# Optimization experiments

Hardware: AMD Instinct MI355X
Metric: run time of the kernel (lower is better)

The kernel has to match this reference:

```python
import jax, jax.numpy as jnp
import numpy as np

D_MODEL = 512
NHEAD = 8


def setup_inputs() -> dict:
    key = jax.random.key(0)
    ks = jax.random.split(key, 8)
    d = D_MODEL
    low_feats = jax.random.normal(ks[0], (1, d, 32, 32), dtype=jnp.float32)
    guide_feats = jax.random.normal(ks[1], (1, d, 128, 128), dtype=jnp.float32)
    s = 1.0 / np.sqrt(d)
    Wq = jax.random.normal(ks[2], (d, d), dtype=jnp.float32) * s
    Wk = jax.random.normal(ks[3], (d, d), dtype=jnp.float32) * s
    Wv = jax.random.normal(ks[4], (d, d), dtype=jnp.float32) * s
    Wm = jax.random.normal(ks[5], (d, d), dtype=jnp.float32) * s
    gamma = jnp.ones((d,), dtype=jnp.float32)
    beta = jnp.zeros((d,), dtype=jnp.float32)
    return {"low_feats": low_feats, "guide_feats": guide_feats, "Wq": Wq,
            "Wk": Wk, "Wv": Wv, "Wm": Wm, "gamma": gamma, "beta": beta}


def _gather_windows(feat_hw, H, W):
    # feat_hw: [b, h, w, nhead, dim]. For each guide pixel (Y,X), nearest low
    # pixel is (Y*h//H, X*w//W) (PyTorch 'nearest'); gather its 3x3 neighborhood
    # with replicate padding (index clamping). Window order = ky*3+kx, matching
    # F.unfold channel layout. Returns [b, H*W, 9, nhead, dim].
    b, h, w, nh, dm = feat_hw.shape
    offs = jnp.array([-1, 0, 1])
    y0 = jnp.arange(H) * h // H                      # [H]
    x0 = jnp.arange(W) * w // W                      # [W]
    ys = jnp.clip(y0[:, None] + offs, 0, h - 1)      # [H,3] (ky)
    xs = jnp.clip(x0[:, None] + offs, 0, w - 1)      # [W,3] (kx)
    # -> [b, H, W, 3(ky), 3(kx), nhead, dim]
    g = feat_hw[:, ys[:, None, :, None], xs[None, :, None, :]]
    return g.reshape(b, H * W, 9, nh, dm)


def reference(low_feats, guide_feats, Wq, Wk, Wv, Wm, gamma, beta):
    b, d, H, W = guide_feats.shape
    _, _, h, w = low_feats.shape
    nh = NHEAD
    dm = d // nh
    g = guide_feats.transpose(0, 2, 3, 1).reshape(b, H * W, d)
    l = low_feats.transpose(0, 2, 3, 1).reshape(b, h * w, d)
    q = (g @ Wq.T).reshape(b, H * W, nh, dm)                 # [b,N,h,d]
    K = (l @ Wk.T).reshape(b, h, w, nh, dm)
    V = (l @ Wv.T).reshape(b, h, w, nh, dm)
    key = _gather_windows(K, H, W)                           # [b,N,9,h,d]
    val = _gather_windows(V, H, W)
    scale = 1.0 / jnp.sqrt(jnp.asarray(dm, dtype=q.dtype))
    # (q/sqrt(dm)) @ (k/sqrt(dm)) * sqrt(dm) == q@k / sqrt(dm)
    score = jnp.einsum('bnhd,bnkhd->bnhk', q, key) * scale
    attn = jax.nn.softmax(score, axis=-1)
    msg = jnp.einsum('bnhk,bnkhd->bnhd', attn, val).reshape(b, H * W, d)
    msg = msg @ Wm.T
    # LayerNorm(d_model), eps=1e-5
    mu = jnp.mean(msg, axis=-1, keepdims=True)
    var = jnp.mean((msg - mu) ** 2, axis=-1, keepdims=True)
    msg = (msg - mu) * jax.lax.rsqrt(var + 1e-5) * gamma + beta
    return msg.transpose(0, 2, 1).reshape(b, d, H, W)
```

## Files before the change

kernel.cpp:

```cpp
#include <hip/hip_runtime.h>
#include <hip/hip_bf16.h>
#include <stdint.h>

#define NQ 16384
#define NL 1024

typedef __bf16 bf16_t;
typedef __bf16 bf16x8 __attribute__((ext_vector_type(8)));
typedef __bf16 bf16x4 __attribute__((ext_vector_type(4)));
typedef float f32x4 __attribute__((ext_vector_type(4)));

__device__ __forceinline__ void gload_lds16(const void* g, void* l) {
  __builtin_amdgcn_global_load_lds(
      (const __attribute__((address_space(1))) uint32_t*)g,
      (__attribute__((address_space(3))) uint32_t*)l, 16, 0, 0);
}

__global__ __launch_bounds__(256) void cvt_all(const float* __restrict__ guide,
                                               const float* __restrict__ low,
                                               const float* __restrict__ Wq,
                                               const float* __restrict__ Wk,
                                               const float* __restrict__ Wv,
                                               const float* __restrict__ Wm,
                                               bf16_t* __restrict__ Gbf,
                                               bf16_t* __restrict__ Lbf,
                                               bf16_t* __restrict__ Wall) {
  const int bx = blockIdx.x, by = blockIdx.y, t = threadIdx.x;
  if (bx >= 544) {
    const int idx = (((bx - 544) * 16 + by) * 256 + t) * 4;
    const float* s;
    int off;
    if (idx < 262144)      { s = Wq; off = idx; }
    else if (idx < 524288) { s = Wk; off = idx - 262144; }
    else if (idx < 786432) { s = Wv; off = idx - 524288; }
    else                   { s = Wm; off = idx - 786432; }
    float4 v = *(const float4*)(s + off);
    bf16x4 o = {(bf16_t)v.x, (bf16_t)v.y, (bf16_t)v.z, (bf16_t)v.w};
    *(bf16x4*)(Wall + idx) = o;
    return;
  }
  __shared__ float tl[32][33];
  const float* src;
  bf16_t* dst;
  int ncols, n0;
  if (bx < 512) { src = guide; dst = Gbf; ncols = NQ; n0 = bx * 32; }
  else          { src = low;   dst = Lbf; ncols = NL; n0 = (bx - 512) * 32; }
  const int c0 = by * 32;
  const int c = t & 31, r = t >> 5;
#pragma unroll
  for (int it = 0; it < 4; ++it) {
    int rr = r + it * 8;
    tl[rr][c] = src[(size_t)(c0 + rr) * ncols + n0 + c];
  }
  __syncthreads();
#pragma unroll
  for (int it = 0; it < 4; ++it) {
    int rr = r + it * 8;
    dst[(size_t)(n0 + rr) * 512 + c0 + c] = (bf16_t)tl[c][rr];
  }
}

__global__ __launch_bounds__(256) void gemm_qkv(const bf16_t* __restrict__ G,
                                                const bf16_t* __restrict__ Wqb,
                                                bf16_t* __restrict__ Qo,
                                                const bf16_t* __restrict__ L,
                                                const bf16_t* __restrict__ Wkv,
                                                bf16_t* __restrict__ KVo) {
  __shared__ __align__(16) bf16_t As[2][128 * 64];
  __shared__ __align__(16) bf16_t Bs[2][128 * 64];
  const bf16_t *A, *B;
  bf16_t* C;
  int N, bm, bn;
  const int bid = blockIdx.x;
  if (bid < 512) { A = G; B = Wqb; C = Qo; N = 512; bm = (bid >> 2) * 128; bn = (bid & 3) * 128; }
  else { int id = bid - 512; A = L; B = Wkv; C = KVo; N = 1024; bm = (id >> 3) * 128; bn = (id & 7) * 128; }
  const int t = threadIdx.x;
  const int lane = t & 63;
  const int wave = t >> 6;
  const int wr = (wave >> 1) * 64;
  const int wc = (wave & 1) * 64;
  const int r0 = t >> 3;
  const int c0 = (t & 7) * 8;
  const int fr = lane & 15;
  const int fk = (lane >> 4) * 8;
#pragma unroll
  for (int it = 0; it < 4; ++it) {
    const int r = r0 + it * 32;
    gload_lds16(A + (size_t)(bm + r) * 512 + c0, &As[0][r * 64 + c0]);
    gload_lds16(B + (size_t)(bn + r) * 512 + c0, &Bs[0][r * 64 + c0]);
  }
  f32x4 acc[4][4] = {};
  __syncthreads();
#pragma unroll 2
  for (int kt = 0; kt < 8; ++kt) {
    const int cur = kt & 1;
    if (kt < 7) {
      const int k0 = (kt + 1) * 64;
#pragma unroll
      for (int it = 0; it < 4; ++it) {
        const int r = r0 + it * 32;
        gload_lds16(A + (size_t)(bm + r) * 512 + k0 + c0, &As[cur ^ 1][r * 64 + c0]);
        gload_lds16(B + (size_t)(bn + r) * 512 + k0 + c0, &Bs[cur ^ 1][r * 64 + c0]);
      }
    }
    __builtin_amdgcn_sched_barrier(0);
#pragma unroll
    for (int kk = 0; kk < 2; ++kk) {
      bf16x8 af[4], bfv[4];
#pragma unroll
      for (int i = 0; i < 4; ++i)
        af[i] = *(const bf16x8*)&As[cur][(wr + i * 16 + fr) * 64 + kk * 32 + fk];
#pragma unroll
      for (int i = 0; i < 4; ++i)
        bfv[i] = *(const bf16x8*)&Bs[cur][(wc + i * 16 + fr) * 64 + kk * 32 + fk];
#pragma unroll
      for (int i = 0; i < 4; ++i)
#pragma unroll
        for (int j = 0; j < 4; ++j)
          acc[i][j] = __builtin_amdgcn_mfma_f32_16x16x32_bf16(af[i], bfv[j], acc[i][j], 0, 0, 0);
    }
    __syncthreads();
  }
  const int crow = bm + wr + ((lane >> 4) * 4);
  const int ccol = bn + wc + fr;
#pragma unroll
  for (int i = 0; i < 4; ++i)
#pragma unroll
    for (int j = 0; j < 4; ++j) {
      const int row = crow + i * 16;
      const int col = ccol + j * 16;
#pragma unroll
      for (int v = 0; v < 4; ++v)
        C[(size_t)(row + v) * N + col] = (bf16_t)acc[i][j][v];
    }
}

__global__ __launch_bounds__(128) void attn_win(const bf16_t* __restrict__ Q,
                                                const bf16_t* __restrict__ KV,
                                                bf16_t* __restrict__ Msg) {
  __shared__ __align__(16) bf16_t Kl[9 * 512];
  __shared__ __align__(16) bf16_t Vl[9 * 512];
  const int t = threadIdx.x;
  const int lane = t & 63;
  const int wave = t >> 6;
  const int tile = blockIdx.x;
  const int ty = tile >> 5, tx = tile & 31;
  for (int kk = wave; kk < 9; kk += 2) {
    int ky = kk / 3, kx = kk - ky * 3;
    int yy = min(max(ty - 1 + ky, 0), 31);
    int xx = min(max(tx - 1 + kx, 0), 31);
    size_t p = (size_t)(yy * 32 + xx) * 1024;
    int dst = kk * 512 + (lane & 7) * 64 + (lane >> 3) * 8;
    *(bf16x8*)&Kl[dst] = *(const bf16x8*)&KV[p + lane * 8];
    *(bf16x8*)&Vl[dst] = *(const bf16x8*)&KV[p + 512 + lane * 8];
  }
  __syncthreads();
  const int pl = t >> 3, h = t & 7;
  const int y = ty * 4 + (pl >> 2), x = tx * 4 + (pl & 3);
  const size_t n = (size_t)y * 128 + x;
  const bf16_t* qrow = Q + n * 512 + h * 64;
  float s[9] = {};
#pragma unroll
  for (int i8 = 0; i8 < 8; ++i8) {
    bf16x8 q8 = *(const bf16x8*)(qrow + i8 * 8);
#pragma unroll
    for (int k = 0; k < 9; ++k) {
      bf16x8 k8 = *(const bf16x8*)&Kl[k * 512 + i8 * 64 + h * 8];
#pragma unroll
      for (int e = 0; e < 8; ++e) s[k] += (float)q8[e] * (float)k8[e];
    }
  }
  float mx = s[0];
#pragma unroll
  for (int k = 1; k < 9; ++k) mx = fmaxf(mx, s[k]);
  float sum = 0.f;
#pragma unroll
  for (int k = 0; k < 9; ++k) {
    s[k] = __expf((s[k] - mx) * 0.125f);
    sum += s[k];
  }
  const float inv = 1.0f / sum;
#pragma unroll
  for (int k = 0; k < 9; ++k) s[k] *= inv;
  bf16_t* orow = Msg + n * 512 + h * 64;
#pragma unroll
  for (int i8 = 0; i8 < 8; ++i8) {
    float accv[8] = {};
#pragma unroll
    for (int k = 0; k < 9; ++k) {
      bf16x8 v8 = *(const bf16x8*)&Vl[k * 512 + i8 * 64 + h * 8];
#pragma unroll
      for (int e = 0; e < 8; ++e) accv[e] += s[k] * (float)v8[e];
    }
    bf16x8 o;
#pragma unroll
    for (int e = 0; e < 8; ++e) o[e] = (bf16_t)accv[e];
    *(bf16x8*)&orow[i8 * 8] = o;
  }
}

__global__ __launch_bounds__(512) void gemm_ln_out(const bf16_t* __restrict__ A,
                                                   const bf16_t* __restrict__ B,
                                                   const float* __restrict__ gamma,
                                                   const float* __restrict__ beta,
                                                   float* __restrict__ out) {
  __shared__ __align__(16) char smem[147456];
  __shared__ float2 part[64][4];
  __shared__ float2 st[64];
  bf16_t* const As0 = (bf16_t*)smem;
  bf16_t* const As1 = (bf16_t*)(smem + 8192);
  bf16_t* const Bs0 = (bf16_t*)(smem + 16384);
  bf16_t* const Bs1 = (bf16_t*)(smem + 81920);
  float* const Cl = (float*)smem;
  const int t = threadIdx.x;
  const int lane = t & 63;
  const int wave = t >> 6;
  const int wr = (wave >> 2) * 32;
  const int wc = (wave & 3) * 128;
  const int bm = blockIdx.x * 64;
  const int sr = t >> 3;
  const int sc = (t & 7) * 8;
  const int fr = lane & 15;
  const int fk = (lane >> 4) * 8;
  gload_lds16(A + (size_t)(bm + sr) * 512 + sc, &As0[sr * 64 + sc]);
#pragma unroll
  for (int it = 0; it < 8; ++it) {
    const int r = sr + it * 64;
    gload_lds16(B + (size_t)r * 512 + sc, &Bs0[r * 64 + sc]);
  }
  f32x4 acc[2][8] = {};
  __syncthreads();
#pragma unroll 2
  for (int kt = 0; kt < 8; ++kt) {
    bf16_t* const Asc = (kt & 1) ? As1 : As0;
    bf16_t* const Bsc = (kt & 1) ? Bs1 : Bs0;
    bf16_t* const Asn = (kt & 1) ? As0 : As1;
    bf16_t* const Bsn = (kt & 1) ? Bs0 : Bs1;
    if (kt < 7) {
      const int k0 = (kt + 1) * 64;
      gload_lds16(A + (size_t)(bm + sr) * 512 + k0 + sc, &Asn[sr * 64 + sc]);
#pragma unroll
      for (int it = 0; it < 8; ++it) {
        const int r = sr + it * 64;
        gload_lds16(B + (size_t)r * 512 + k0 + sc, &Bsn[r * 64 + sc]);
      }
    }
    __builtin_amdgcn_sched_barrier(0);
#pragma unroll
    for (int kk = 0; kk < 2; ++kk) {
      bf16x8 af[2], bfv[8];
#pragma unroll
      for (int i = 0; i < 2; ++i)
        af[i] = *(const bf16x8*)&Asc[(wr + i * 16 + fr) * 64 + kk * 32 + fk];
#pragma unroll
      for (int j = 0; j < 8; ++j)
        bfv[j] = *(const bf16x8*)&Bsc[(wc + j * 16 + fr) * 64 + kk * 32 + fk];
#pragma unroll
      for (int i = 0; i < 2; ++i)
#pragma unroll
        for (int j = 0; j < 8; ++j)
          acc[i][j] = __builtin_amdgcn_mfma_f32_16x16x32_bf16(af[i], bfv[j], acc[i][j], 0, 0, 0);
    }
    __syncthreads();
  }
#pragma unroll
  for (int i = 0; i < 2; ++i)
#pragma unroll
    for (int j = 0; j < 8; ++j) {
      const int row = wr + i * 16 + (lane >> 4) * 4;
      const int col = wc + j * 16 + fr;
#pragma unroll
      for (int v = 0; v < 4; ++v) Cl[(row + v) * 513 + col] = acc[i][j][v];
    }
#pragma unroll
  for (int i = 0; i < 2; ++i)
#pragma unroll
    for (int v = 0; v < 4; ++v) {
      float s = 0.f, s2 = 0.f;
#pragma unroll
      for (int j = 0; j < 8; ++j) {
        float x = acc[i][j][v];
        s += x;
        s2 += x * x;
      }
#pragma unroll
      for (int m = 1; m < 16; m <<= 1) {
        s += __shfl_xor(s, m, 64);
        s2 += __shfl_xor(s2, m, 64);
      }
      if ((lane & 15) == 0) {
        const int row = wr + i * 16 + (lane >> 4) * 4 + v;
        part[row][wave & 3] = make_float2(s, s2);
      }
    }
  __syncthreads();
  if (t < 64) {
    float2 p0 = part[t][0], p1 = part[t][1], p2 = part[t][2], p3 = part[t][3];
    float s = p0.x + p1.x + p2.x + p3.x;
    float s2 = p0.y + p1.y + p2.y + p3.y;
    float mu = s * (1.f / 512.f);
    float var = s2 * (1.f / 512.f) - mu * mu;
    st[t] = make_float2(mu, rsqrtf(var + 1e-5f));
  }
  __syncthreads();
  const int n = t & 63;
  const int j0 = t >> 6;
  const float2 ms = st[n];
#pragma unroll 8
  for (int jj = 0; jj < 64; ++jj) {
    const int j = j0 * 64 + jj;
    const float g = gamma[j], b = beta[j];
    const float x = Cl[n * 513 + j];
    out[(size_t)j * NQ + bm + n] = (x - ms.x) * ms.y * g + b;
  }
}

extern "C" void kernel_launch(void* const* d_in, const int* in_sizes, int n_in,
                              void* d_out, int out_size, void* d_ws, size_t ws_size,
                              hipStream_t stream) {
  const float* low = (const float*)d_in[0];
  const float* guide = (const float*)d_in[1];
  const float* Wq = (const float*)d_in[2];
  const float* Wk = (const float*)d_in[3];
  const float* Wv = (const float*)d_in[4];
  const float* Wm = (const float*)d_in[5];
  const float* gamma = (const float*)d_in[6];
  const float* beta = (const float*)d_in[7];
  float* out = (float*)d_out;

  char* w = (char*)d_ws;
  bf16_t* Gbf = (bf16_t*)w;  w += (size_t)NQ * 512 * 2;
  bf16_t* Lbf = (bf16_t*)w;  w += (size_t)NL * 512 * 2;
  bf16_t* Wall = (bf16_t*)w; w += (size_t)4 * 512 * 512 * 2;
  bf16_t* Qbf = (bf16_t*)w;  w += (size_t)NQ * 512 * 2;
  bf16_t* KVbf = (bf16_t*)w; w += (size_t)NL * 1024 * 2;
  bf16_t* Msg = (bf16_t*)w;  w += (size_t)NQ * 512 * 2;

  cvt_all<<<dim3(608, 16), 256, 0, stream>>>(guide, low, Wq, Wk, Wv, Wm, Gbf, Lbf, Wall);
  gemm_qkv<<<dim3(576), 256, 0, stream>>>(Gbf, Wall, Qbf, Lbf, Wall + 262144, KVbf);
  attn_win<<<dim3(1024), 128, 0, stream>>>(Qbf, KVbf, Msg);
  gemm_ln_out<<<dim3(NQ / 64), 512, 0, stream>>>(Msg, Wall + 786432, gamma, beta, out);
}
```

Measured before the change: 168.9 us.

## Split each attention head across four lanes with shuffle reductions in window attention

The window-attention kernel now uses 512 threads per block, with four lanes sharing each (pixel, head) pair. Each lane handles 16 of the 64 head dimensions, and the dot-product partial sums are combined with xor shuffles. The K/V shared-memory layout becomes a plain contiguous copy, and each lane's Q loads and Msg stores become two 16-byte accesses to neighbouring memory instead of eight strided ones. This is meant to raise parallelism and improve memory coalescing in the memory-bound attention step, at the cost of the shuffle reductions and repeating the softmax on every lane.

```diff
diff --git a/kernel.cpp b/kernel.cpp
--- a/kernel.cpp
+++ b/kernel.cpp
@@ -135,7 +135,7 @@
     }
 }
 
-__global__ __launch_bounds__(128) void attn_win(const bf16_t* __restrict__ Q,
+__global__ __launch_bounds__(512) void attn_win(const bf16_t* __restrict__ Q,
                                                 const bf16_t* __restrict__ KV,
                                                 bf16_t* __restrict__ Msg) {
   __shared__ __align__(16) bf16_t Kl[9 * 512];
@@ -145,30 +145,34 @@
   const int wave = t >> 6;
   const int tile = blockIdx.x;
   const int ty = tile >> 5, tx = tile & 31;
-  for (int kk = wave; kk < 9; kk += 2) {
+  for (int kk = wave; kk < 9; kk += 8) {
     int ky = kk / 3, kx = kk - ky * 3;
     int yy = min(max(ty - 1 + ky, 0), 31);
     int xx = min(max(tx - 1 + kx, 0), 31);
     size_t p = (size_t)(yy * 32 + xx) * 1024;
-    int dst = kk * 512 + (lane & 7) * 64 + (lane >> 3) * 8;
-    *(bf16x8*)&Kl[dst] = *(const bf16x8*)&KV[p + lane * 8];
-    *(bf16x8*)&Vl[dst] = *(const bf16x8*)&KV[p + 512 + lane * 8];
-  }
-  __syncthreads();
-  const int pl = t >> 3, h = t & 7;
+    *(bf16x8*)&Kl[kk * 512 + lane * 8] = *(const bf16x8*)&KV[p + lane * 8];
+    *(bf16x8*)&Vl[kk * 512 + lane * 8] = *(const bf16x8*)&KV[p + 512 + lane * 8];
+  }
+  __syncthreads();
+  const int c = t & 3;
+  const int h = (t >> 2) & 7;
+  const int pl = t >> 5;
   const int y = ty * 4 + (pl >> 2), x = tx * 4 + (pl & 3);
   const size_t n = (size_t)y * 128 + x;
-  const bf16_t* qrow = Q + n * 512 + h * 64;
-  float s[9] = {};
-#pragma unroll
-  for (int i8 = 0; i8 < 8; ++i8) {
-    bf16x8 q8 = *(const bf16x8*)(qrow + i8 * 8);
-#pragma unroll
-    for (int k = 0; k < 9; ++k) {
-      bf16x8 k8 = *(const bf16x8*)&Kl[k * 512 + i8 * 64 + h * 8];
-#pragma unroll
-      for (int e = 0; e < 8; ++e) s[k] += (float)q8[e] * (float)k8[e];
-    }
+  const int doff = h * 64 + c * 16;
+  const bf16x8 q0 = *(const bf16x8*)(Q + n * 512 + doff);
+  const bf16x8 q1 = *(const bf16x8*)(Q + n * 512 + doff + 8);
+  float s[9];
+#pragma unroll
+  for (int k = 0; k < 9; ++k) {
+    bf16x8 k0 = *(const bf16x8*)&Kl[k * 512 + doff];
+    bf16x8 k1 = *(const bf16x8*)&Kl[k * 512 + doff + 8];
+    float p = 0.f;
+#pragma unroll
+    for (int e = 0; e < 8; ++e) p += (float)q0[e] * (float)k0[e] + (float)q1[e] * (float)k1[e];
+    p += __shfl_xor(p, 1, 64);
+    p += __shfl_xor(p, 2, 64);
+    s[k] = p;
   }
   float mx = s[0];
 #pragma unroll
@@ -180,23 +184,23 @@
     sum += s[k];
   }
   const float inv = 1.0f / sum;
-#pragma unroll
-  for (int k = 0; k < 9; ++k) s[k] *= inv;
-  bf16_t* orow = Msg + n * 512 + h * 64;
-#pragma unroll
-  for (int i8 = 0; i8 < 8; ++i8) {
-    float accv[8] = {};
-#pragma unroll
-    for (int k = 0; k < 9; ++k) {
-      bf16x8 v8 = *(const bf16x8*)&Vl[k * 512 + i8 * 64 + h * 8];
-#pragma unroll
-      for (int e = 0; e < 8; ++e) accv[e] += s[k] * (float)v8[e];
-    }
-    bf16x8 o;
-#pragma unroll
-    for (int e = 0; e < 8; ++e) o[e] = (bf16_t)accv[e];
-    *(bf16x8*)&orow[i8 * 8] = o;
-  }
+  float acc[16] = {};
+#pragma unroll
+  for (int k = 0; k < 9; ++k) {
+    const float p = s[k] * inv;
+    bf16x8 v0 = *(const bf16x8*)&Vl[k * 512 + doff];
+    bf16x8 v1 = *(const bf16x8*)&Vl[k * 512 + doff + 8];
+#pragma unroll
+    for (int e = 0; e < 8; ++e) {
+      acc[e] += p * (float)v0[e];
+      acc[8 + e] += p * (float)v1[e];
+    }
+  }
+  bf16x8 o0, o1;
+#pragma unroll
+  for (int e = 0; e < 8; ++e) { o0[e] = (bf16_t)acc[e]; o1[e] = (bf16_t)acc[8 + e]; }
+  *(bf16x8*)(Msg + n * 512 + doff) = o0;
+  *(bf16x8*)(Msg + n * 512 + doff + 8) = o1;
 }
 
 __global__ __launch_bounds__(512) void gemm_ln_out(const bf16_t* __restrict__ A,
@@ -338,6 +342,6 @@
 
   cvt_all<<<dim3(608, 16), 256, 0, stream>>>(guide, low, Wq, Wk, Wv, Wm, Gbf, Lbf, Wall);
   gemm_qkv<<<dim3(576), 256, 0, stream>>>(Gbf, Wall, Qbf, Lbf, Wall + 262144, KVbf);
-  attn_win<<<dim3(1024), 128, 0, stream>>>(Qbf, KVbf, Msg);
+  attn_win<<<dim3(1024), 512, 0, stream>>>(Qbf, KVbf, Msg);
   gemm_ln_out<<<dim3(NQ / 64), 512, 0, stream>>>(Msg, Wall + 786432, gamma, beta, out);
 }
```

Measured after the change: 165.9 us. Within noise of the previous version (-1.7%).
